# Performance work log

Hardware: AMD Instinct MI355X
Metric: run time of the kernel (lower is better)

Reference implementation:

```python
import jax, jax.numpy as jnp
import numpy as np

H = 8  # hidden_size

def setup_inputs() -> dict:
    key = jax.random.key(0)
    ks = jax.random.split(key, 7)
    B, T, I = 131072, 48, 5
    s = 1.0 / np.sqrt(H)  # torch LSTM/Linear init scale (uniform bound); use scaled normal
    return {
        "x": jax.random.normal(ks[0], (B, T, I), dtype=jnp.float32),
        "W_ih": jax.random.normal(ks[1], (4 * H, I), dtype=jnp.float32) * s,
        "W_hh": jax.random.normal(ks[2], (4 * H, H), dtype=jnp.float32) * s,
        "b_ih": jax.random.normal(ks[3], (4 * H,), dtype=jnp.float32) * s,
        "b_hh": jax.random.normal(ks[4], (4 * H,), dtype=jnp.float32) * s,
        "fc_W": jax.random.normal(ks[5], (1, H * T), dtype=jnp.float32) * (1.0 / np.sqrt(H * T)),
        "fc_b": jax.random.normal(ks[6], (1,), dtype=jnp.float32) * (1.0 / np.sqrt(H * T)),
    }

def _lstm_forward(x, W_ih, W_hh, b_ih, b_hh):
    # x: [B, T, I]. PyTorch gate order: i, f, g, o.
    B, T, _ = x.shape
    # Precompute input projections for all timesteps: [B, T, 4H] -> [T, B, 4H]
    xp = jnp.einsum('bti,gi->btg', x, W_ih) + b_ih + b_hh
    xp = xp.transpose(1, 0, 2)

    def step(carry, xt):
        h, c = carry
        gates = xt + h @ W_hh.T  # [B, 4H]
        i, f, g, o = jnp.split(gates, 4, axis=-1)
        c = jax.nn.sigmoid(f) * c + jax.nn.sigmoid(i) * jnp.tanh(g)
        h = jax.nn.sigmoid(o) * jnp.tanh(c)
        return (h, c), h

    h0 = jnp.zeros((B, H), dtype=x.dtype)
    c0 = jnp.zeros((B, H), dtype=x.dtype)
    _, hs = jax.lax.scan(step, (h0, c0), xp)  # hs: [T, B, H]
    return hs.transpose(1, 0, 2)  # [B, T, H]

def reference(x, W_ih, W_hh, b_ih, b_hh, fc_W, fc_b):
    B, T, _ = x.shape
    lstm_out = _lstm_forward(x, W_ih, W_hh, b_ih, b_hh)  # [B, T, H]
    preds = lstm_out.reshape(B, T * H) @ fc_W.T + fc_b   # [B, 1]
    return preds.reshape(-1)  # [B]
```

## Files before the change

kernel.cpp:

```cpp
#include <hip/hip_runtime.h>

#define TT 48
#define II 5
#define HID 8

typedef float float2v __attribute__((ext_vector_type(2)));

template<int CTRL>
__device__ __forceinline__ float dppf(float v) {
    return __int_as_float(__builtin_amdgcn_update_dpp(0, __float_as_int(v), CTRL, 0xF, 0xF, true));
}

__device__ __forceinline__ float fexp2(float x) {
    float r; asm("v_exp_f32 %0, %1" : "=v"(r) : "v"(x)); return r;
}
__device__ __forceinline__ float frcp(float x) { return __builtin_amdgcn_rcpf(x); }
__device__ __forceinline__ float2v pkfma(float2v a, float2v b, float2v c) {
    return __builtin_elementwise_fma(a, b, c);
}
__device__ __forceinline__ float2v splat(float v) { return (float2v){v, v}; }
__device__ __forceinline__ void pin2(float2v& v) { asm("" : "+v"(v)); }

__global__ __launch_bounds__(256, 4) void lstm_fused(
    const float* __restrict__ x,
    const float* __restrict__ W_ih,
    const float* __restrict__ W_hh,
    const float* __restrict__ b_ih,
    const float* __restrict__ b_hh,
    const float* __restrict__ fc_W,
    const float* __restrict__ fc_b,
    float* __restrict__ out, int B)
{
    __shared__ __align__(16) float s_fc[TT * HID];
    const int tid = threadIdx.x;
    for (int i = tid; i < TT * HID; i += 256) s_fc[i] = fc_W[i];
    __syncthreads();

    const int gt = blockIdx.x * 256 + tid;
    const int b = gt >> 3;
    const int q = gt & 7;
    if (b >= B) return;

    const float L2E  = 1.44269504088896340736f;
    const float L2E2 = 2.0f * L2E;
    const float sI = -L2E, sF = -L2E, sG = L2E2, sO = -L2E;

    const int r_i = q, r_f = 8 + q, r_g = 16 + q, r_o = 24 + q;

    float2v wihA[II], wihB[II], whhA[HID], whhB[HID], biasA, biasB;
    #pragma unroll
    for (int i = 0; i < II; ++i) {
        wihA[i] = (float2v){sI * W_ih[r_i * II + i], sF * W_ih[r_f * II + i]};
        wihB[i] = (float2v){sG * W_ih[r_g * II + i], sO * W_ih[r_o * II + i]};
    }
    #pragma unroll
    for (int m = 0; m < HID; ++m) {
        const int e = q ^ m;
        whhA[m] = (float2v){sI * W_hh[r_i * HID + e], sF * W_hh[r_f * HID + e]};
        whhB[m] = (float2v){sG * W_hh[r_g * HID + e], sO * W_hh[r_o * HID + e]};
    }
    biasA = (float2v){sI * (b_ih[r_i] + b_hh[r_i]), sF * (b_ih[r_f] + b_hh[r_f])};
    biasB = (float2v){sG * (b_ih[r_g] + b_hh[r_g]), sO * (b_ih[r_o] + b_hh[r_o])};

    #pragma unroll
    for (int i = 0; i < II; ++i) { pin2(wihA[i]); pin2(wihB[i]); }
    #pragma unroll
    for (int m = 0; m < HID; ++m) { pin2(whhA[m]); pin2(whhB[m]); }
    pin2(biasA); pin2(biasB);

    const float* xb = x + (size_t)b * (TT * II);
    const float4* xb4 = reinterpret_cast<const float4*>(xb);

    float h = 0.f, c = 0.f, acc = 0.f;

    float xc[20];
    #pragma unroll
    for (int k = 0; k < 5; ++k) {
        float4 v = xb4[k];
        xc[4*k] = v.x; xc[4*k+1] = v.y; xc[4*k+2] = v.z; xc[4*k+3] = v.w;
    }

    #pragma unroll 1
    for (int bi = 0; bi < 12; ++bi) {
        const int nb = (bi < 11) ? bi + 1 : 11;
        float4 p[5];
        #pragma unroll
        for (int k = 0; k < 5; ++k) p[k] = xb4[nb * 5 + k];

        #pragma unroll
        for (int s = 0; s < 4; ++s) {
            const int t = bi * 4 + s;

            float2v gA = pkfma(wihA[0], splat(xc[s*5 + 0]), biasA);
            float2v gB = pkfma(wihB[0], splat(xc[s*5 + 0]), biasB);
            #pragma unroll
            for (int i = 1; i < II; ++i) {
                gA = pkfma(wihA[i], splat(xc[s*5 + i]), gA);
                gB = pkfma(wihB[i], splat(xc[s*5 + i]), gB);
            }

            const float ha1 = dppf<0xB1>(h);
            const float ha2 = dppf<0x4E>(h);
            const float ha3 = dppf<0x1B>(h);
            const float ha7 = dppf<0x141>(h);
            const float ha6 = dppf<0x141>(ha1);
            const float ha5 = dppf<0x141>(ha2);
            const float ha4 = dppf<0x141>(ha3);

            gA = pkfma(whhA[0], splat(h),   gA);  gB = pkfma(whhB[0], splat(h),   gB);
            gA = pkfma(whhA[1], splat(ha1), gA);  gB = pkfma(whhB[1], splat(ha1), gB);
            gA = pkfma(whhA[2], splat(ha2), gA);  gB = pkfma(whhB[2], splat(ha2), gB);
            gA = pkfma(whhA[3], splat(ha3), gA);  gB = pkfma(whhB[3], splat(ha3), gB);
            gA = pkfma(whhA[4], splat(ha4), gA);  gB = pkfma(whhB[4], splat(ha4), gB);
            gA = pkfma(whhA[5], splat(ha5), gA);  gB = pkfma(whhB[5], splat(ha5), gB);
            gA = pkfma(whhA[6], splat(ha6), gA);  gB = pkfma(whhB[6], splat(ha6), gB);
            gA = pkfma(whhA[7], splat(ha7), gA);  gB = pkfma(whhB[7], splat(ha7), gB);

            const float si = frcp(1.0f + fexp2(gA.x));
            const float sf = frcp(1.0f + fexp2(gA.y));
            const float tg = fmaf(-2.0f, frcp(1.0f + fexp2(gB.x)), 1.0f);
            const float so = frcp(1.0f + fexp2(gB.y));

            c = fmaf(sf, c, si * tg);
            const float tc = fmaf(-2.0f, frcp(1.0f + fexp2(c * L2E2)), 1.0f);
            h = so * tc;

            acc = fmaf(h, s_fc[t * HID + q], acc);
        }

        #pragma unroll
        for (int k = 0; k < 5; ++k) {
            xc[4*k] = p[k].x; xc[4*k+1] = p[k].y; xc[4*k+2] = p[k].z; xc[4*k+3] = p[k].w;
        }
    }

    acc += dppf<0xB1>(acc);
    acc += dppf<0x4E>(acc);
    acc += dppf<0x141>(acc);
    if (q == 0) out[b] = acc + fc_b[0];
}

extern "C" void kernel_launch(void* const* d_in, const int* in_sizes, int n_in,
                              void* d_out, int out_size, void* d_ws, size_t ws_size,
                              hipStream_t stream) {
    const float* x    = (const float*)d_in[0];
    const float* W_ih = (const float*)d_in[1];
    const float* W_hh = (const float*)d_in[2];
    const float* b_ih = (const float*)d_in[3];
    const float* b_hh = (const float*)d_in[4];
    const float* fc_W = (const float*)d_in[5];
    const float* fc_b = (const float*)d_in[6];
    float* out = (float*)d_out;

    const int B = in_sizes[0] / (TT * II);
    const long long threads = (long long)B * 8;
    const int grid = (int)((threads + 255) / 256);
    lstm_fused<<<grid, 256, 0, stream>>>(x, W_ih, W_hh, b_ih, b_hh, fc_W, fc_b, out, B);
}
```

Measured before the change: 105.6 us.

## Process two batch rows per 8-lane group with packed FMA across rows

Each 8-lane group now handles two batch elements at once. Its packed FMAs put the two rows in the two halves of each register, and inline-asm op_sel picks the weight half, so the gate weights are shared across rows. This halves the thread count and aims to raise useful work per instruction and interleave two independent recurrence chains to hide latency. In exchange, the scalar transcendental work per thread doubles, register pressure rises (launch bounds drop to 3 waves), and the kernel now assumes B is even.

```diff
diff --git a/kernel.cpp b/kernel.cpp
--- a/kernel.cpp
+++ b/kernel.cpp
@@ -10,18 +10,27 @@
 __device__ __forceinline__ float dppf(float v) {
     return __int_as_float(__builtin_amdgcn_update_dpp(0, __float_as_int(v), CTRL, 0xF, 0xF, true));
 }
-
 __device__ __forceinline__ float fexp2(float x) {
     float r; asm("v_exp_f32 %0, %1" : "=v"(r) : "v"(x)); return r;
 }
 __device__ __forceinline__ float frcp(float x) { return __builtin_amdgcn_rcpf(x); }
-__device__ __forceinline__ float2v pkfma(float2v a, float2v b, float2v c) {
-    return __builtin_elementwise_fma(a, b, c);
+
+__device__ __forceinline__ float2v pk_lo(float2v acc, float2v w, float2v x) {
+    asm("v_pk_fma_f32 %0, %1, %2, %0 op_sel_hi:[0,1,1]" : "+v"(acc) : "v"(w), "v"(x));
+    return acc;
 }
-__device__ __forceinline__ float2v splat(float v) { return (float2v){v, v}; }
+__device__ __forceinline__ float2v pk_hi(float2v acc, float2v w, float2v x) {
+    asm("v_pk_fma_f32 %0, %1, %2, %0 op_sel:[1,0,0] op_sel_hi:[1,1,1]" : "+v"(acc) : "v"(w), "v"(x));
+    return acc;
+}
+__device__ __forceinline__ float2v pk_lo3(float2v w, float2v x, float2v b) {
+    float2v d;
+    asm("v_pk_fma_f32 %0, %1, %2, %3 op_sel_hi:[0,1,1]" : "=v"(d) : "v"(w), "v"(x), "v"(b));
+    return d;
+}
 __device__ __forceinline__ void pin2(float2v& v) { asm("" : "+v"(v)); }
 
-__global__ __launch_bounds__(256, 4) void lstm_fused(
+__global__ __launch_bounds__(256, 3) void lstm_fused(
     const float* __restrict__ x,
     const float* __restrict__ W_ih,
     const float* __restrict__ W_hh,
@@ -37,107 +46,118 @@
     __syncthreads();
 
     const int gt = blockIdx.x * 256 + tid;
-    const int b = gt >> 3;
+    const int grp = gt >> 3;
     const int q = gt & 7;
-    if (b >= B) return;
+    const int b0 = grp * 2;
+    if (b0 >= B) return;
 
     const float L2E  = 1.44269504088896340736f;
     const float L2E2 = 2.0f * L2E;
-    const float sI = -L2E, sF = -L2E, sG = L2E2, sO = -L2E;
+    const float sc[4] = {-L2E, -L2E, L2E2, -L2E};
 
-    const int r_i = q, r_f = 8 + q, r_g = 16 + q, r_o = 24 + q;
-
-    float2v wihA[II], wihB[II], whhA[HID], whhB[HID], biasA, biasB;
+    float2v wih[4][2], w4p[2], whh[4][4], biasp[4];
     #pragma unroll
-    for (int i = 0; i < II; ++i) {
-        wihA[i] = (float2v){sI * W_ih[r_i * II + i], sF * W_ih[r_f * II + i]};
-        wihB[i] = (float2v){sG * W_ih[r_g * II + i], sO * W_ih[r_o * II + i]};
+    for (int g = 0; g < 4; ++g) {
+        const int row = g * HID + q;
+        wih[g][0] = (float2v){sc[g] * W_ih[row * II + 0], sc[g] * W_ih[row * II + 1]};
+        wih[g][1] = (float2v){sc[g] * W_ih[row * II + 2], sc[g] * W_ih[row * II + 3]};
+        #pragma unroll
+        for (int j = 0; j < 4; ++j)
+            whh[g][j] = (float2v){sc[g] * W_hh[row * HID + (q ^ (2 * j))],
+                                  sc[g] * W_hh[row * HID + (q ^ (2 * j + 1))]};
+        const float bb = sc[g] * (b_ih[row] + b_hh[row]);
+        biasp[g] = (float2v){bb, bb};
     }
-    #pragma unroll
-    for (int m = 0; m < HID; ++m) {
-        const int e = q ^ m;
-        whhA[m] = (float2v){sI * W_hh[r_i * HID + e], sF * W_hh[r_f * HID + e]};
-        whhB[m] = (float2v){sG * W_hh[r_g * HID + e], sO * W_hh[r_o * HID + e]};
-    }
-    biasA = (float2v){sI * (b_ih[r_i] + b_hh[r_i]), sF * (b_ih[r_f] + b_hh[r_f])};
-    biasB = (float2v){sG * (b_ih[r_g] + b_hh[r_g]), sO * (b_ih[r_o] + b_hh[r_o])};
+    w4p[0] = (float2v){sc[0] * W_ih[(0 * HID + q) * II + 4], sc[1] * W_ih[(1 * HID + q) * II + 4]};
+    w4p[1] = (float2v){sc[2] * W_ih[(2 * HID + q) * II + 4], sc[3] * W_ih[(3 * HID + q) * II + 4]};
 
     #pragma unroll
-    for (int i = 0; i < II; ++i) { pin2(wihA[i]); pin2(wihB[i]); }
+    for (int g = 0; g < 4; ++g) {
+        pin2(wih[g][0]); pin2(wih[g][1]); pin2(biasp[g]);
+        #pragma unroll
+        for (int j = 0; j < 4; ++j) pin2(whh[g][j]);
+    }
+    pin2(w4p[0]); pin2(w4p[1]);
+
+    const float2* xA = reinterpret_cast<const float2*>(x + (size_t)b0 * (TT * II));
+    const float2* xB = reinterpret_cast<const float2*>(x + (size_t)(b0 + 1) * (TT * II));
+
+    float2 pA[5], pB[5];
     #pragma unroll
-    for (int m = 0; m < HID; ++m) { pin2(whhA[m]); pin2(whhB[m]); }
-    pin2(biasA); pin2(biasB);
+    for (int k = 0; k < 5; ++k) { pA[k] = xA[k]; pB[k] = xB[k]; }
 
-    const float* xb = x + (size_t)b * (TT * II);
-    const float4* xb4 = reinterpret_cast<const float4*>(xb);
-
-    float h = 0.f, c = 0.f, acc = 0.f;
-
-    float xc[20];
-    #pragma unroll
-    for (int k = 0; k < 5; ++k) {
-        float4 v = xb4[k];
-        xc[4*k] = v.x; xc[4*k+1] = v.y; xc[4*k+2] = v.z; xc[4*k+3] = v.w;
-    }
+    float2v c01 = (float2v){0.f, 0.f}, h01 = (float2v){0.f, 0.f};
+    float accA = 0.f, accB = 0.f;
 
     #pragma unroll 1
-    for (int bi = 0; bi < 12; ++bi) {
-        const int nb = (bi < 11) ? bi + 1 : 11;
-        float4 p[5];
+    for (int ch = 0; ch < 24; ++ch) {
+        float2v xp[10];
         #pragma unroll
-        for (int k = 0; k < 5; ++k) p[k] = xb4[nb * 5 + k];
+        for (int k = 0; k < 5; ++k) {
+            xp[2 * k]     = (float2v){pA[k].x, pB[k].x};
+            xp[2 * k + 1] = (float2v){pA[k].y, pB[k].y};
+        }
+        const int nc = (ch < 23) ? ch + 1 : 23;
+        #pragma unroll
+        for (int k = 0; k < 5; ++k) { pA[k] = xA[nc * 5 + k]; pB[k] = xB[nc * 5 + k]; }
 
         #pragma unroll
-        for (int s = 0; s < 4; ++s) {
-            const int t = bi * 4 + s;
+        for (int s = 0; s < 2; ++s) {
+            const int t = ch * 2 + s;
+            const float2v* xs = &xp[s * 5];
 
-            float2v gA = pkfma(wihA[0], splat(xc[s*5 + 0]), biasA);
-            float2v gB = pkfma(wihB[0], splat(xc[s*5 + 0]), biasB);
+            float2v hap1 = (float2v){dppf<0xB1>(h01.x),  dppf<0xB1>(h01.y)};
+            float2v hap2 = (float2v){dppf<0x4E>(h01.x),  dppf<0x4E>(h01.y)};
+            float2v hap3 = (float2v){dppf<0x1B>(h01.x),  dppf<0x1B>(h01.y)};
+            float2v hap7 = (float2v){dppf<0x141>(h01.x), dppf<0x141>(h01.y)};
+            float2v hap6 = (float2v){dppf<0x141>(hap1.x), dppf<0x141>(hap1.y)};
+            float2v hap5 = (float2v){dppf<0x141>(hap2.x), dppf<0x141>(hap2.y)};
+            float2v hap4 = (float2v){dppf<0x141>(hap3.x), dppf<0x141>(hap3.y)};
+
+            float2v gg[4];
             #pragma unroll
-            for (int i = 1; i < II; ++i) {
-                gA = pkfma(wihA[i], splat(xc[s*5 + i]), gA);
-                gB = pkfma(wihB[i], splat(xc[s*5 + i]), gB);
+            for (int g = 0; g < 4; ++g) {
+                float2v a = pk_lo3(wih[g][0], xs[0], biasp[g]);
+                a = pk_hi(a, wih[g][0], xs[1]);
+                a = pk_lo(a, wih[g][1], xs[2]);
+                a = pk_hi(a, wih[g][1], xs[3]);
+                a = (g & 1) ? pk_hi(a, w4p[g >> 1], xs[4]) : pk_lo(a, w4p[g >> 1], xs[4]);
+                a = pk_lo(a, whh[g][0], h01);
+                a = pk_hi(a, whh[g][0], hap1);
+                a = pk_lo(a, whh[g][1], hap2);
+                a = pk_hi(a, whh[g][1], hap3);
+                a = pk_lo(a, whh[g][2], hap4);
+                a = pk_hi(a, whh[g][2], hap5);
+                a = pk_lo(a, whh[g][3], hap6);
+                a = pk_hi(a, whh[g][3], hap7);
+                gg[g] = a;
             }
 
-            const float ha1 = dppf<0xB1>(h);
-            const float ha2 = dppf<0x4E>(h);
-            const float ha3 = dppf<0x1B>(h);
-            const float ha7 = dppf<0x141>(h);
-            const float ha6 = dppf<0x141>(ha1);
-            const float ha5 = dppf<0x141>(ha2);
-            const float ha4 = dppf<0x141>(ha3);
+            const float si0 = frcp(1.f + fexp2(gg[0].x)), si1 = frcp(1.f + fexp2(gg[0].y));
+            const float sf0 = frcp(1.f + fexp2(gg[1].x)), sf1 = frcp(1.f + fexp2(gg[1].y));
+            const float tg0 = fmaf(-2.f, frcp(1.f + fexp2(gg[2].x)), 1.f);
+            const float tg1 = fmaf(-2.f, frcp(1.f + fexp2(gg[2].y)), 1.f);
+            const float so0 = frcp(1.f + fexp2(gg[3].x)), so1 = frcp(1.f + fexp2(gg[3].y));
 
-            gA = pkfma(whhA[0], splat(h),   gA);  gB = pkfma(whhB[0], splat(h),   gB);
-            gA = pkfma(whhA[1], splat(ha1), gA);  gB = pkfma(whhB[1], splat(ha1), gB);
-            gA = pkfma(whhA[2], splat(ha2), gA);  gB = pkfma(whhB[2], splat(ha2), gB);
-            gA = pkfma(whhA[3], splat(ha3), gA);  gB = pkfma(whhB[3], splat(ha3), gB);
-            gA = pkfma(whhA[4], splat(ha4), gA);  gB = pkfma(whhB[4], splat(ha4), gB);
-            gA = pkfma(whhA[5], splat(ha5), gA);  gB = pkfma(whhB[5], splat(ha5), gB);
-            gA = pkfma(whhA[6], splat(ha6), gA);  gB = pkfma(whhB[6], splat(ha6), gB);
-            gA = pkfma(whhA[7], splat(ha7), gA);  gB = pkfma(whhB[7], splat(ha7), gB);
+            c01.x = fmaf(sf0, c01.x, si0 * tg0);
+            c01.y = fmaf(sf1, c01.y, si1 * tg1);
+            const float tc0 = fmaf(-2.f, frcp(1.f + fexp2(c01.x * L2E2)), 1.f);
+            const float tc1 = fmaf(-2.f, frcp(1.f + fexp2(c01.y * L2E2)), 1.f);
+            h01.x = so0 * tc0;
+            h01.y = so1 * tc1;
 
-            const float si = frcp(1.0f + fexp2(gA.x));
-            const float sf = frcp(1.0f + fexp2(gA.y));
-            const float tg = fmaf(-2.0f, frcp(1.0f + fexp2(gB.x)), 1.0f);
-            const float so = frcp(1.0f + fexp2(gB.y));
-
-            c = fmaf(sf, c, si * tg);
-            const float tc = fmaf(-2.0f, frcp(1.0f + fexp2(c * L2E2)), 1.0f);
-            h = so * tc;
-
-            acc = fmaf(h, s_fc[t * HID + q], acc);
-        }
-
-        #pragma unroll
-        for (int k = 0; k < 5; ++k) {
-            xc[4*k] = p[k].x; xc[4*k+1] = p[k].y; xc[4*k+2] = p[k].z; xc[4*k+3] = p[k].w;
+            const float fcw = s_fc[t * HID + q];
+            accA = fmaf(h01.x, fcw, accA);
+            accB = fmaf(h01.y, fcw, accB);
         }
     }
 
-    acc += dppf<0xB1>(acc);
-    acc += dppf<0x4E>(acc);
-    acc += dppf<0x141>(acc);
-    if (q == 0) out[b] = acc + fc_b[0];
+    accA += dppf<0xB1>(accA); accA += dppf<0x4E>(accA); accA += dppf<0x141>(accA);
+    accB += dppf<0xB1>(accB); accB += dppf<0x4E>(accB); accB += dppf<0x141>(accB);
+    if (q == 0) {
+        float2 o2 = {accA + fc_b[0], accB + fc_b[0]};
+        *reinterpret_cast<float2*>(out + b0) = o2;
+    }
 }
 
 extern "C" void kernel_launch(void* const* d_in, const int* in_sizes, int n_in,
@@ -153,7 +173,7 @@
     float* out = (float*)d_out;
 
     const int B = in_sizes[0] / (TT * II);
-    const long long threads = (long long)B * 8;
+    const long long threads = (long long)(B / 2) * 8;
     const int grid = (int)((threads + 255) / 256);
     lstm_fused<<<grid, 256, 0, stream>>>(x, W_ih, W_hh, b_ih, b_hh, fc_W, fc_b, out, B);
 }
```

New measurement: 105.6 us. Within noise of the previous version (+0.0%).
